# Kernel tuning notes

Measured on AMD Instinct MI355X. Metric: run time of the kernel, lower is better.

The kernel has to match this reference:

```python
import jax, jax.numpy as jnp
import numpy as np

SEG_LEN = 64
SIG_LEN = 1056
NUM_SEG = 32
STEP = 32  # segment_length * (1 - overlap)

# flat scatter indices: position of element j of segment i in the output signal
_IDX = (np.arange(NUM_SEG)[:, None] * STEP + np.arange(SEG_LEN)[None, :]).reshape(-1)


def combine_segments(segments):
    # segments: (B, C, NUM_SEG, SEG_LEN) -> (B, C, SIG_LEN) overlap-add then normalize
    B, C = segments.shape[0], segments.shape[1]
    idx = jnp.asarray(_IDX)
    out = jnp.zeros((B, C, SIG_LEN), segments.dtype).at[:, :, idx].add(
        segments.reshape(B, C, NUM_SEG * SEG_LEN))
    counter = jnp.zeros((SIG_LEN,), segments.dtype).at[idx].add(1.0)
    return out / counter  # broadcast over (B, C)


def setup_inputs() -> dict:
    key = jax.random.key(0)
    ks = jax.random.split(key, 9)
    B, C, T, E, H = 1024, 8, 32, 128, 256
    s = lambda k, shape, fan: jax.random.normal(k, shape, jnp.float32) * (1.0 / np.sqrt(fan))
    return {
        "encoder_output": jax.random.normal(ks[0], (B, C, T, E), jnp.float32),
        "W1": s(ks[1], (H, E), E), "b1": s(ks[2], (H,), E),
        "W2": s(ks[3], (E, H), H), "b2": s(ks[4], (E,), H),
        "Winv": s(ks[5], (SEG_LEN, E), E), "binv": s(ks[6], (SEG_LEN,), E),
        "Wconv": s(ks[7], (1, C, 3), C * 3), "bconv": s(ks[8], (1,), C * 3),
    }


def reference(encoder_output, W1, b1, W2, b2, Winv, binv, Wconv, bconv):
    # MLP: Linear -> ReLU -> Linear over embedding dim
    h = jax.nn.relu(jnp.einsum('bcte,he->bcth', encoder_output, W1) + b1)
    x = jnp.einsum('bcth,eh->bcte', h, W2) + b2
    # inverse token embedding: E -> SEG_LEN
    x = jnp.einsum('bcte,se->bcts', x, Winv) + binv  # (B, C, T, SEG_LEN)
    # overlap-add reconstruction + normalization
    x = combine_segments(x)  # (B, C, SIG_LEN)
    # ChannelMerger: Conv1d(C -> 1, k=3, padding=1)
    y = jax.lax.conv_general_dilated(
        x, Wconv, window_strides=(1,), padding=[(1, 1)],
        dimension_numbers=('NCH', 'OIH', 'NCH'))
    return y + bconv[None, :, None]
```

## Files before the change

### kernel.cpp

```cpp
#include <hip/hip_runtime.h>
#include <hip/hip_bf16.h>


typedef __bf16 bf16x8 __attribute__((ext_vector_type(8)));
typedef float  f32x4  __attribute__((ext_vector_type(4)));
typedef unsigned int u32;
typedef u32 u32x2 __attribute__((ext_vector_type(2)));

#define L_W1   0
#define L_HS   65536
#define L_SGA  102400
#define L_SGB  119424
#define L_B1   136448
#define L_BC   137472
#define L_WV   137728
#define LDS_SZ 137856

#define BAR_LDS() do {                                              \
    __builtin_amdgcn_sched_barrier(0);                              \
    asm volatile("s_waitcnt lgkmcnt(0)" ::: "memory");              \
    __builtin_amdgcn_s_barrier();                                   \
    __builtin_amdgcn_sched_barrier(0);                              \
  } while (0)

static __device__ __forceinline__ bf16x8 cvt8(f32x4 a, f32x4 b) {
  bf16x8 r;
  r[0] = (__bf16)a[0]; r[1] = (__bf16)a[1]; r[2] = (__bf16)a[2]; r[3] = (__bf16)a[3];
  r[4] = (__bf16)b[0]; r[5] = (__bf16)b[1]; r[6] = (__bf16)b[2]; r[7] = (__bf16)b[3];
  return r;
}
static __device__ __forceinline__ u32 packbf2(float a, float b) {
  union { __hip_bfloat16 h; unsigned short s; } ua, ub;
  ua.h = __float2bfloat16(a); ub.h = __float2bfloat16(b);
  return (u32)ua.s | ((u32)ub.s << 16);
}
static __device__ __forceinline__ float lo16f(u32 w) { return __uint_as_float(w << 16); }
static __device__ __forceinline__ float hi16f(u32 w) { return __uint_as_float(w & 0xffff0000u); }

__global__ __launch_bounds__(256) void k_precomp(
    const float* __restrict__ W2, const float* __restrict__ b2,
    const float* __restrict__ Winv, const float* __restrict__ binv,
    __hip_bfloat16* __restrict__ Wcpre, float* __restrict__ bc) {
  __shared__ float wrow[128];
  const int s = blockIdx.x, h = threadIdx.x;
  if (h < 128) wrow[h] = Winv[s * 128 + h];
  __syncthreads();
  float acc = 0.f;
  #pragma unroll 8
  for (int e = 0; e < 128; ++e) acc = fmaf(wrow[e], W2[e * 256 + h], acc);
  const int nc = h >> 6, ks2 = (h >> 5) & 1, g = (h >> 3) & 3, j = h & 7;
  const int nt2 = s >> 4, q = s & 15;
  Wcpre[((((nc * 2 + ks2) * 4 + nt2) * 4 + g) * 16 + q) * 8 + j] = __float2bfloat16(acc);
  if (h == 0) {
    float a = binv[s];
    for (int e = 0; e < 128; ++e) a = fmaf(wrow[e], b2[e], a);
    bc[s] = a;
  }
}

__global__ __launch_bounds__(512)
__attribute__((amdgpu_waves_per_eu(2, 2)))
void k_gemm(const float* __restrict__ X,
            const float* __restrict__ W1,
            const float* __restrict__ b1,
            const __hip_bfloat16* __restrict__ Wcpre,
            const float* __restrict__ bcp,
            const float* __restrict__ Wcv,
            const float* __restrict__ bcv,
            float* __restrict__ Out)
{
  extern __shared__ __align__(16) char smem[];
  const int tid = threadIdx.x;
  const int wave = tid >> 6, lane = tid & 63;
  const int q = lane & 15, g = lane >> 4;
  const int c = wave;
  const int b0 = blockIdx.x * 4;

  f32x4 xa[16];
  #define LOADX(bb) do {                                                        \
    _Pragma("unroll")                                                           \
    for (int _mt = 0; _mt < 2; ++_mt) {                                         \
      const float* _s = X + ((size_t)((bb) * 8 + c)) * 4096                     \
                          + (_mt * 16 + q) * 128 + g * 8;                       \
      _Pragma("unroll")                                                         \
      for (int _ks = 0; _ks < 4; ++_ks) {                                       \
        xa[(_mt * 4 + _ks) * 2 + 0] = *reinterpret_cast<const f32x4*>(_s + _ks * 32);     \
        xa[(_mt * 4 + _ks) * 2 + 1] = *reinterpret_cast<const f32x4*>(_s + _ks * 32 + 4); \
      } } } while (0)

  LOADX(b0);

  #pragma unroll
  for (int i = 0; i < 8; ++i) {
    const int p8 = tid + i * 512;
    const int fq = p8 & 15, fg = (p8 >> 4) & 3, fks = (p8 >> 6) & 3;
    const int fnt = (p8 >> 8) & 3, fnc = (p8 >> 10) & 3;
    const float* src = W1 + (fnc * 64 + fnt * 16 + fq) * 128 + fks * 32 + fg * 8;
    *reinterpret_cast<bf16x8*>(smem + L_W1 + p8 * 16) =
        cvt8(*reinterpret_cast<const f32x4*>(src),
             *reinterpret_cast<const f32x4*>(src + 4));
  }
  {
    if (tid < 256)               ((float*)(smem + L_B1))[tid]       = b1[tid];
    if (tid >= 256 && tid < 320) ((float*)(smem + L_BC))[tid - 256] = bcp[tid - 256];
    if (tid >= 320 && tid < 344) ((float*)(smem + L_WV))[tid - 320] = Wcv[tid - 320];
    if (tid == 344)              ((float*)(smem + L_WV))[24]        = bcv[0];
    if (tid >= 384 && tid < 448) {
      const int t = tid - 384, buf = t >> 5, cc = (t & 31) >> 2, k = t & 3;
      *reinterpret_cast<u32*>(
          reinterpret_cast<__hip_bfloat16*>(smem + (buf ? L_SGB : L_SGA))
          + cc * 1064 + 1056 + 2 * k) = 0u;
    }
  }
  BAR_LDS();

  __hip_bfloat16* Hb = reinterpret_cast<__hip_bfloat16*>(smem + L_HS) + wave * 2304;
  const float* smB1 = (const float*)(smem + L_B1);
  const float* smBC = (const float*)(smem + L_BC);
  const float* smWV = (const float*)(smem + L_WV);

  #pragma unroll 1
  for (int it = 0; it < 4; ++it) {
    bf16x8 af[2][4];
    #pragma unroll
    for (int f = 0; f < 8; ++f) af[f >> 2][f & 3] = cvt8(xa[2 * f], xa[2 * f + 1]);

    f32x4 acc2[2][4] = {};

    #pragma unroll 1
    for (int nc = 0; nc < 4; ++nc) {
      bf16x8 bw2f[2][4];
      #pragma unroll
      for (int ks2 = 0; ks2 < 2; ++ks2)
        #pragma unroll
        for (int nt2 = 0; nt2 < 4; ++nt2)
          bw2f[ks2][nt2] = *reinterpret_cast<const bf16x8*>(
              Wcpre + ((nc * 2 + ks2) * 4 + nt2) * 512 + lane * 8);

      f32x4 acc1[2][4] = {};
      #pragma unroll
      for (int ks = 0; ks < 4; ++ks) {
        bf16x8 bw[4];
        #pragma unroll
        for (int nt = 0; nt < 4; ++nt)
          bw[nt] = *reinterpret_cast<const bf16x8*>(
              smem + L_W1 + (((nc * 4 + nt) * 4 + ks) << 10) + lane * 16);
        __builtin_amdgcn_s_setprio(1);
        #pragma unroll
        for (int nt = 0; nt < 4; ++nt) {
          acc1[0][nt] = __builtin_amdgcn_mfma_f32_16x16x32_bf16(bw[nt], af[0][ks], acc1[0][nt], 0, 0, 0);
          acc1[1][nt] = __builtin_amdgcn_mfma_f32_16x16x32_bf16(bw[nt], af[1][ks], acc1[1][nt], 0, 0, 0);
        }
        __builtin_amdgcn_s_setprio(0);
      }
      #pragma unroll
      for (int nt = 0; nt < 4; ++nt) {
        const f32x4 b1q = *reinterpret_cast<const f32x4*>(smB1 + nc * 64 + nt * 16 + 4 * g);
        #pragma unroll
        for (int mt = 0; mt < 2; ++mt) {
          u32x2 w;
          w[0] = packbf2(fmaxf(acc1[mt][nt][0] + b1q[0], 0.f),
                         fmaxf(acc1[mt][nt][1] + b1q[1], 0.f));
          w[1] = packbf2(fmaxf(acc1[mt][nt][2] + b1q[2], 0.f),
                         fmaxf(acc1[mt][nt][3] + b1q[3], 0.f));
          *reinterpret_cast<u32x2*>(Hb + (mt * 16 + q) * 72 + nt * 16 + 4 * g) = w;
        }
      }
      #pragma unroll
      for (int ks2 = 0; ks2 < 2; ++ks2) {
        bf16x8 bh[2];
        #pragma unroll
        for (int mt = 0; mt < 2; ++mt)
          bh[mt] = *reinterpret_cast<const bf16x8*>(Hb + (mt * 16 + q) * 72 + ks2 * 32 + g * 8);
        __builtin_amdgcn_s_setprio(1);
        #pragma unroll
        for (int nt2 = 0; nt2 < 4; ++nt2) {
          acc2[0][nt2] = __builtin_amdgcn_mfma_f32_16x16x32_bf16(bw2f[ks2][nt2], bh[0], acc2[0][nt2], 0, 0, 0);
          acc2[1][nt2] = __builtin_amdgcn_mfma_f32_16x16x32_bf16(bw2f[ks2][nt2], bh[1], acc2[1][nt2], 0, 0, 0);
        }
        __builtin_amdgcn_s_setprio(0);
      }
    }

    if (it < 3) LOADX(b0 + it + 1);

    __hip_bfloat16* Sl = Hb;
    #pragma unroll
    for (int nt2 = 0; nt2 < 4; ++nt2) {
      const f32x4 bcq = *reinterpret_cast<const f32x4*>(smBC + nt2 * 16 + 4 * g);
      #pragma unroll
      for (int mt = 0; mt < 2; ++mt) {
        u32x2 w;
        w[0] = packbf2(acc2[mt][nt2][0] + bcq[0], acc2[mt][nt2][1] + bcq[1]);
        w[1] = packbf2(acc2[mt][nt2][2] + bcq[2], acc2[mt][nt2][3] + bcq[3]);
        *reinterpret_cast<u32x2*>(Sl + (mt * 16 + q) * 68 + nt2 * 16 + 4 * g) = w;
      }
    }

    {
      __hip_bfloat16* sigc = reinterpret_cast<__hip_bfloat16*>(
          smem + ((it & 1) ? L_SGB : L_SGA)) + c * 1064;
      #pragma unroll
      for (int w = 0; w < 5; ++w) {
        const int u = w * 64 + lane;
        if (u < 264) {
          const int p = 4 * u, t = p >> 5, j = p & 31;
          u32x2 r1 = {0u, 0u}, r2 = {0u, 0u};
          if (t < 32) r1 = *reinterpret_cast<const u32x2*>(Sl + t * 68 + j);
          if (t > 0)  r2 = *reinterpret_cast<const u32x2*>(Sl + (t - 1) * 68 + j + 32);
          const float nrm = (t == 0 || t == 32) ? 1.f : 0.5f;
          u32x2 wv;
          wv[0] = packbf2(nrm * (lo16f(r1[0]) + lo16f(r2[0])),
                          nrm * (hi16f(r1[0]) + hi16f(r2[0])));
          wv[1] = packbf2(nrm * (lo16f(r1[1]) + lo16f(r2[1])),
                          nrm * (hi16f(r1[1]) + hi16f(r2[1])));
          *reinterpret_cast<u32x2*>(sigc + p) = wv;
        }
      }
    }

    if (it & 1) {
      BAR_LDS();
      const float bconv = smWV[24];
      #pragma unroll 1
      for (int rr = 0; rr < 2; ++rr) {
        const int u = tid + rr * 512;
        if (u < 528) {
          const int half = (u >= 264) ? 1 : 0;
          const __hip_bfloat16* sg = reinterpret_cast<const __hip_bfloat16*>(
              smem + (half ? L_SGB : L_SGA));
          const int p0 = (u - half * 264) * 4;
          f32x4 acc = {bconv, bconv, bconv, bconv};
          #pragma unroll
          for (int cc = 0; cc < 8; ++cc) {
            const __hip_bfloat16* row = sg + cc * 1064;
            const u32 wm = (p0 > 0) ? *reinterpret_cast<const u32*>(row + p0 - 2) : 0u;
            const u32x2 wc = *reinterpret_cast<const u32x2*>(row + p0);
            const u32 wr = *reinterpret_cast<const u32*>(row + p0 + 4);
            const float l  = hi16f(wm);
            const float a0 = lo16f(wc[0]), a1 = hi16f(wc[0]);
            const float a2 = lo16f(wc[1]), a3 = hi16f(wc[1]);
            const float r  = lo16f(wr);
            const float w0 = smWV[cc * 3], w1 = smWV[cc * 3 + 1], w2 = smWV[cc * 3 + 2];
            acc[0] = fmaf(w0, l,  fmaf(w1, a0, fmaf(w2, a1, acc[0])));
            acc[1] = fmaf(w0, a0, fmaf(w1, a1, fmaf(w2, a2, acc[1])));
            acc[2] = fmaf(w0, a1, fmaf(w1, a2, fmaf(w2, a3, acc[2])));
            acc[3] = fmaf(w0, a2, fmaf(w1, a3, fmaf(w2, r,  acc[3])));
          }
          *reinterpret_cast<f32x4*>(
              Out + (size_t)(b0 + it - 1 + half) * 1056 + p0) = acc;
        }
      }
      if (it != 3) BAR_LDS();
    }
  }
  #undef LOADX
}

extern "C" void kernel_launch(void* const* d_in, const int* in_sizes, int n_in,
                              void* d_out, int out_size, void* d_ws, size_t ws_size,
                              hipStream_t stream) {
  const float* X    = (const float*)d_in[0];
  const float* W1   = (const float*)d_in[1];
  const float* b1   = (const float*)d_in[2];
  const float* W2   = (const float*)d_in[3];
  const float* b2   = (const float*)d_in[4];
  const float* Winv = (const float*)d_in[5];
  const float* binv = (const float*)d_in[6];
  const float* Wcv  = (const float*)d_in[7];
  const float* bcv  = (const float*)d_in[8];

  __hip_bfloat16* Wcpre = (__hip_bfloat16*)((char*)d_ws + 65536);
  float*          bcp   = (float*)((char*)d_ws + 98304);

  k_precomp<<<64, 256, 0, stream>>>(W2, b2, Winv, binv, Wcpre, bcp);
  k_gemm<<<256, 512, LDS_SZ, stream>>>(X, W1, b1, Wcpre, bcp, Wcv, bcv,
                                       (float*)d_out);
}
```

Before: 58.96 us.

## Split fused GEMM into small-block GEMM plus separate conv kernel via workspace

Replaces the single large-LDS 512-thread kernel (256 blocks, one per 4 batches) with a 2048-block kernel that does MLP+projection+overlap-add per (batch, half of channels) and writes the bf16 signal to workspace, followed by a separate conv kernel. W1 is pre-converted to bf16 in MFMA fragment order in the precompute kernel and read directly from global/L2 instead of staged in LDS. The aim is to raise occupancy and parallelism by dropping the large LDS footprint and cross-channel synchronization, at the cost of an extra kernel launch, an intermediate bf16 round-trip through memory, and an additional bf16 rounding of the signal. The old fused path stays as a fallback when the workspace is too small.

```diff
diff --git a/kernel.cpp b/kernel.cpp
--- a/kernel.cpp
+++ b/kernel.cpp
@@ -16,6 +16,11 @@
 #define L_WV   137728
 #define LDS_SZ 137856
 
+#define LA_HS  0
+#define LA_B1  18432
+#define LA_BC  19456
+#define LA_SZ  19712
+
 #define BAR_LDS() do {                                              \
     __builtin_amdgcn_sched_barrier(0);                              \
     asm volatile("s_waitcnt lgkmcnt(0)" ::: "memory");              \
@@ -38,11 +43,22 @@
 static __device__ __forceinline__ float hi16f(u32 w) { return __uint_as_float(w & 0xffff0000u); }
 
 __global__ __launch_bounds__(256) void k_precomp(
+    const float* __restrict__ W1,
     const float* __restrict__ W2, const float* __restrict__ b2,
     const float* __restrict__ Winv, const float* __restrict__ binv,
-    __hip_bfloat16* __restrict__ Wcpre, float* __restrict__ bc) {
+    __hip_bfloat16* __restrict__ Wcpre, __hip_bfloat16* __restrict__ W1pre,
+    float* __restrict__ bc) {
   __shared__ float wrow[128];
   const int s = blockIdx.x, h = threadIdx.x;
+  if (h < 64) {
+    const int p8 = s * 64 + h;
+    const int fq = p8 & 15, fg = (p8 >> 4) & 3, fks = (p8 >> 6) & 3;
+    const int fnt = (p8 >> 8) & 3, fnc = (p8 >> 10) & 3;
+    const float* src = W1 + (fnc * 64 + fnt * 16 + fq) * 128 + fks * 32 + fg * 8;
+    *reinterpret_cast<bf16x8*>(W1pre + p8 * 8) =
+        cvt8(*reinterpret_cast<const f32x4*>(src),
+             *reinterpret_cast<const f32x4*>(src + 4));
+  }
   if (h < 128) wrow[h] = Winv[s * 128 + h];
   __syncthreads();
   float acc = 0.f;
@@ -58,17 +74,182 @@
   }
 }
 
+__global__ __launch_bounds__(256)
+void k_gemm_s(const float* __restrict__ X,
+              const __hip_bfloat16* __restrict__ W1p,
+              const float* __restrict__ b1,
+              const __hip_bfloat16* __restrict__ Wcpre,
+              const float* __restrict__ bcp,
+              __hip_bfloat16* __restrict__ Sig)
+{
+  __shared__ __align__(16) char smem[LA_SZ];
+  const int tid = threadIdx.x;
+  const int wave = tid >> 6, lane = tid & 63;
+  const int q = lane & 15, g = lane >> 4;
+  const int b = blockIdx.x >> 1, cq = blockIdx.x & 1;
+  const int c = cq * 4 + wave;
+
+  f32x4 xa[16];
+  {
+    const float* xs = X + ((size_t)(b * 8 + c)) * 4096;
+    #pragma unroll
+    for (int mt = 0; mt < 2; ++mt)
+      #pragma unroll
+      for (int ks = 0; ks < 4; ++ks) {
+        const float* s = xs + (mt * 16 + q) * 128 + ks * 32 + g * 8;
+        xa[(mt * 4 + ks) * 2 + 0] = *reinterpret_cast<const f32x4*>(s);
+        xa[(mt * 4 + ks) * 2 + 1] = *reinterpret_cast<const f32x4*>(s + 4);
+      }
+  }
+
+  if (tid < 256) ((float*)(smem + LA_B1))[tid] = b1[tid];
+  if (tid < 64)  ((float*)(smem + LA_BC))[tid] = bcp[tid];
+  BAR_LDS();
+
+  __hip_bfloat16* Hb = reinterpret_cast<__hip_bfloat16*>(smem + LA_HS) + wave * 2304;
+  const float* smB1 = (const float*)(smem + LA_B1);
+  const float* smBC = (const float*)(smem + LA_BC);
+
+  bf16x8 af[2][4];
+  #pragma unroll
+  for (int f = 0; f < 8; ++f) af[f >> 2][f & 3] = cvt8(xa[2 * f], xa[2 * f + 1]);
+
+  f32x4 acc2[2][4] = {};
+
+  #pragma unroll 1
+  for (int nc = 0; nc < 4; ++nc) {
+    f32x4 acc1[2][4] = {};
+    #pragma unroll
+    for (int ks = 0; ks < 4; ++ks) {
+      bf16x8 bw[4];
+      #pragma unroll
+      for (int nt = 0; nt < 4; ++nt)
+        bw[nt] = *reinterpret_cast<const bf16x8*>(
+            W1p + (((nc * 4 + nt) * 4 + ks) << 9) + lane * 8);
+      __builtin_amdgcn_s_setprio(1);
+      #pragma unroll
+      for (int nt = 0; nt < 4; ++nt) {
+        acc1[0][nt] = __builtin_amdgcn_mfma_f32_16x16x32_bf16(bw[nt], af[0][ks], acc1[0][nt], 0, 0, 0);
+        acc1[1][nt] = __builtin_amdgcn_mfma_f32_16x16x32_bf16(bw[nt], af[1][ks], acc1[1][nt], 0, 0, 0);
+      }
+      __builtin_amdgcn_s_setprio(0);
+    }
+    #pragma unroll
+    for (int nt = 0; nt < 4; ++nt) {
+      const f32x4 b1q = *reinterpret_cast<const f32x4*>(smB1 + nc * 64 + nt * 16 + 4 * g);
+      #pragma unroll
+      for (int mt = 0; mt < 2; ++mt) {
+        u32x2 w;
+        w[0] = packbf2(fmaxf(acc1[mt][nt][0] + b1q[0], 0.f),
+                       fmaxf(acc1[mt][nt][1] + b1q[1], 0.f));
+        w[1] = packbf2(fmaxf(acc1[mt][nt][2] + b1q[2], 0.f),
+                       fmaxf(acc1[mt][nt][3] + b1q[3], 0.f));
+        *reinterpret_cast<u32x2*>(Hb + (mt * 16 + q) * 72 + nt * 16 + 4 * g) = w;
+      }
+    }
+    #pragma unroll
+    for (int ks2 = 0; ks2 < 2; ++ks2) {
+      bf16x8 bh[2];
+      #pragma unroll
+      for (int mt = 0; mt < 2; ++mt)
+        bh[mt] = *reinterpret_cast<const bf16x8*>(Hb + (mt * 16 + q) * 72 + ks2 * 32 + g * 8);
+      bf16x8 bw2[4];
+      #pragma unroll
+      for (int nt2 = 0; nt2 < 4; ++nt2)
+        bw2[nt2] = *reinterpret_cast<const bf16x8*>(
+            Wcpre + ((nc * 2 + ks2) * 4 + nt2) * 512 + lane * 8);
+      __builtin_amdgcn_s_setprio(1);
+      #pragma unroll
+      for (int nt2 = 0; nt2 < 4; ++nt2) {
+        acc2[0][nt2] = __builtin_amdgcn_mfma_f32_16x16x32_bf16(bw2[nt2], bh[0], acc2[0][nt2], 0, 0, 0);
+        acc2[1][nt2] = __builtin_amdgcn_mfma_f32_16x16x32_bf16(bw2[nt2], bh[1], acc2[1][nt2], 0, 0, 0);
+      }
+      __builtin_amdgcn_s_setprio(0);
+    }
+  }
+
+  __hip_bfloat16* Sl = Hb;
+  #pragma unroll
+  for (int nt2 = 0; nt2 < 4; ++nt2) {
+    const f32x4 bcq = *reinterpret_cast<const f32x4*>(smBC + nt2 * 16 + 4 * g);
+    #pragma unroll
+    for (int mt = 0; mt < 2; ++mt) {
+      u32x2 w;
+      w[0] = packbf2(acc2[mt][nt2][0] + bcq[0], acc2[mt][nt2][1] + bcq[1]);
+      w[1] = packbf2(acc2[mt][nt2][2] + bcq[2], acc2[mt][nt2][3] + bcq[3]);
+      *reinterpret_cast<u32x2*>(Sl + (mt * 16 + q) * 68 + nt2 * 16 + 4 * g) = w;
+    }
+  }
+
+  {
+    __hip_bfloat16* sigc = Sig + (size_t)(b * 8 + c) * 1056;
+    #pragma unroll
+    for (int w = 0; w < 5; ++w) {
+      const int u = w * 64 + lane;
+      if (u < 264) {
+        const int p = 4 * u, t = p >> 5, j = p & 31;
+        u32x2 r1 = {0u, 0u}, r2 = {0u, 0u};
+        if (t < 32) r1 = *reinterpret_cast<const u32x2*>(Sl + t * 68 + j);
+        if (t > 0)  r2 = *reinterpret_cast<const u32x2*>(Sl + (t - 1) * 68 + j + 32);
+        const float nrm = (t == 0 || t == 32) ? 1.f : 0.5f;
+        u32x2 wv;
+        wv[0] = packbf2(nrm * (lo16f(r1[0]) + lo16f(r2[0])),
+                        nrm * (hi16f(r1[0]) + hi16f(r2[0])));
+        wv[1] = packbf2(nrm * (lo16f(r1[1]) + lo16f(r2[1])),
+                        nrm * (hi16f(r1[1]) + hi16f(r2[1])));
+        *reinterpret_cast<u32x2*>(sigc + p) = wv;
+      }
+    }
+  }
+}
+
+__global__ __launch_bounds__(256)
+void k_conv(const __hip_bfloat16* __restrict__ Sig,
+            const float* __restrict__ Wcv, const float* __restrict__ bcv,
+            float* __restrict__ Out) {
+  __shared__ float wv[25];
+  if (threadIdx.x < 24) wv[threadIdx.x] = Wcv[threadIdx.x];
+  if (threadIdx.x == 24) wv[24] = bcv[0];
+  __syncthreads();
+  const int b = blockIdx.x;
+  const float bconv = wv[24];
+  #pragma unroll 1
+  for (int rr = 0; rr < 2; ++rr) {
+    const int u = threadIdx.x + rr * 256;
+    if (u < 264) {
+      const int p0 = 4 * u;
+      f32x4 acc = {bconv, bconv, bconv, bconv};
+      #pragma unroll
+      for (int cc = 0; cc < 8; ++cc) {
+        const __hip_bfloat16* row = Sig + (size_t)(b * 8 + cc) * 1056;
+        const u32 wm = (p0 > 0) ? *reinterpret_cast<const u32*>(row + p0 - 2) : 0u;
+        const u32x2 wc = *reinterpret_cast<const u32x2*>(row + p0);
+        const u32 wr = (p0 + 4 < 1056) ? *reinterpret_cast<const u32*>(row + p0 + 4) : 0u;
+        const float l  = hi16f(wm);
+        const float a0 = lo16f(wc[0]), a1 = hi16f(wc[0]);
+        const float a2 = lo16f(wc[1]), a3 = hi16f(wc[1]);
+        const float r  = lo16f(wr);
+        const float w0 = wv[cc * 3], w1 = wv[cc * 3 + 1], w2 = wv[cc * 3 + 2];
+        acc[0] = fmaf(w0, l,  fmaf(w1, a0, fmaf(w2, a1, acc[0])));
+        acc[1] = fmaf(w0, a0, fmaf(w1, a1, fmaf(w2, a2, acc[1])));
+        acc[2] = fmaf(w0, a1, fmaf(w1, a2, fmaf(w2, a3, acc[2])));
+        acc[3] = fmaf(w0, a2, fmaf(w1, a3, fmaf(w2, r,  acc[3])));
+      }
+      *reinterpret_cast<f32x4*>(Out + (size_t)b * 1056 + p0) = acc;
+    }
+  }
+}
+
 __global__ __launch_bounds__(512)
 __attribute__((amdgpu_waves_per_eu(2, 2)))
-void k_gemm(const float* __restrict__ X,
-            const float* __restrict__ W1,
-            const float* __restrict__ b1,
-            const __hip_bfloat16* __restrict__ Wcpre,
-            const float* __restrict__ bcp,
-            const float* __restrict__ Wcv,
-            const float* __restrict__ bcv,
-            float* __restrict__ Out)
-{
+void k_gemm_fused(const float* __restrict__ X,
+                  const float* __restrict__ W1,
+                  const float* __restrict__ b1,
+                  const __hip_bfloat16* __restrict__ Wcpre,
+                  const float* __restrict__ bcp,
+                  const float* __restrict__ Wcv,
+                  const float* __restrict__ bcv,
+                  float* __restrict__ Out) {
   extern __shared__ __align__(16) char smem[];
   const int tid = threadIdx.x;
   const int wave = tid >> 6, lane = tid & 63;
@@ -270,10 +451,18 @@
   const float* Wcv  = (const float*)d_in[7];
   const float* bcv  = (const float*)d_in[8];
 
+  __hip_bfloat16* W1pre = (__hip_bfloat16*)d_ws;
   __hip_bfloat16* Wcpre = (__hip_bfloat16*)((char*)d_ws + 65536);
   float*          bcp   = (float*)((char*)d_ws + 98304);
-
-  k_precomp<<<64, 256, 0, stream>>>(W2, b2, Winv, binv, Wcpre, bcp);
-  k_gemm<<<256, 512, LDS_SZ, stream>>>(X, W1, b1, Wcpre, bcp, Wcv, bcv,
-                                       (float*)d_out);
-}
+  __hip_bfloat16* Sig   = (__hip_bfloat16*)((char*)d_ws + 131072);
+  const size_t need = 131072 + (size_t)1024 * 8 * 1056 * 2;
+
+  k_precomp<<<64, 256, 0, stream>>>(W1, W2, b2, Winv, binv, Wcpre, W1pre, bcp);
+  if (ws_size >= need) {
+    k_gemm_s<<<2048, 256, 0, stream>>>(X, W1pre, b1, Wcpre, bcp, Sig);
+    k_conv<<<1024, 256, 0, stream>>>(Sig, Wcv, bcv, (float*)d_out);
+  } else {
+    k_gemm_fused<<<256, 512, LDS_SZ, stream>>>(X, W1, b1, Wcpre, bcp, Wcv, bcv,
+                                               (float*)d_out);
+  }
+}
```

New measurement: 83.40 us. 41.4% more time.

## Software-pipeline fused MLP chunk loop to overlap GEMM1 of next chunk with GEMM2

Applied to the files above, without the earlier changes.

Restructures the per-chunk hidden-dimension loop into a software pipeline: the H tile for chunk nc is written and read back, then GEMM1 for chunk nc+1 is issued before GEMM2 for chunk nc, and the W2 fragments for the next chunk are prefetched afterwards. The aim is to hide the LDS write/read latency of the hidden activations and the global W2 loads behind independent MFMA work. In exchange, more accumulators and fragments are live at once, which raises register pressure and could reduce occupancy or cause spills.

```diff
diff --git a/kernel.cpp b/kernel.cpp
--- a/kernel.cpp
+++ b/kernel.cpp
@@ -119,6 +119,77 @@
   const float* smBC = (const float*)(smem + L_BC);
   const float* smWV = (const float*)(smem + L_WV);
 
+  #define LOADW2(ncx) do {                                                      \
+    _Pragma("unroll")                                                           \
+    for (int _k = 0; _k < 2; ++_k)                                              \
+      _Pragma("unroll")                                                         \
+      for (int _n = 0; _n < 4; ++_n)                                            \
+        bw2f[_k][_n] = *reinterpret_cast<const bf16x8*>(                        \
+            Wcpre + (((ncx) * 2 + _k) * 4 + _n) * 512 + lane * 8);              \
+  } while (0)
+
+  #define GEMM1(ncx) do {                                                       \
+    _Pragma("unroll")                                                           \
+    for (int _m = 0; _m < 2; ++_m)                                              \
+      _Pragma("unroll")                                                         \
+      for (int _n = 0; _n < 4; ++_n)                                            \
+        acc1[_m][_n] = (f32x4){0.f, 0.f, 0.f, 0.f};                             \
+    _Pragma("unroll")                                                           \
+    for (int _ks = 0; _ks < 4; ++_ks) {                                         \
+      bf16x8 _bw[4];                                                            \
+      _Pragma("unroll")                                                         \
+      for (int _n = 0; _n < 4; ++_n)                                            \
+        _bw[_n] = *reinterpret_cast<const bf16x8*>(                             \
+            smem + L_W1 + ((((ncx) * 4 + _n) * 4 + _ks) << 10) + lane * 16);    \
+      __builtin_amdgcn_s_setprio(1);                                            \
+      _Pragma("unroll")                                                         \
+      for (int _n = 0; _n < 4; ++_n) {                                          \
+        acc1[0][_n] = __builtin_amdgcn_mfma_f32_16x16x32_bf16(_bw[_n], af[0][_ks], acc1[0][_n], 0, 0, 0); \
+        acc1[1][_n] = __builtin_amdgcn_mfma_f32_16x16x32_bf16(_bw[_n], af[1][_ks], acc1[1][_n], 0, 0, 0); \
+      }                                                                         \
+      __builtin_amdgcn_s_setprio(0);                                            \
+    }                                                                           \
+  } while (0)
+
+  #define HWRITE(ncx) do {                                                      \
+    _Pragma("unroll")                                                           \
+    for (int _n = 0; _n < 4; ++_n) {                                            \
+      const f32x4 _b1q = *reinterpret_cast<const f32x4*>(                       \
+          smB1 + (ncx) * 64 + _n * 16 + 4 * g);                                 \
+      _Pragma("unroll")                                                         \
+      for (int _m = 0; _m < 2; ++_m) {                                          \
+        u32x2 _w;                                                               \
+        _w[0] = packbf2(fmaxf(acc1[_m][_n][0] + _b1q[0], 0.f),                  \
+                        fmaxf(acc1[_m][_n][1] + _b1q[1], 0.f));                 \
+        _w[1] = packbf2(fmaxf(acc1[_m][_n][2] + _b1q[2], 0.f),                  \
+                        fmaxf(acc1[_m][_n][3] + _b1q[3], 0.f));                 \
+        *reinterpret_cast<u32x2*>(Hb + (_m * 16 + q) * 72 + _n * 16 + 4 * g) = _w; \
+      }                                                                         \
+    }                                                                           \
+  } while (0)
+
+  #define BHREAD() do {                                                         \
+    _Pragma("unroll")                                                           \
+    for (int _k = 0; _k < 2; ++_k)                                              \
+      _Pragma("unroll")                                                         \
+      for (int _m = 0; _m < 2; ++_m)                                            \
+        bh[_k][_m] = *reinterpret_cast<const bf16x8*>(                          \
+            Hb + (_m * 16 + q) * 72 + _k * 32 + g * 8);                         \
+  } while (0)
+
+  #define GEMM2() do {                                                          \
+    _Pragma("unroll")                                                           \
+    for (int _k = 0; _k < 2; ++_k) {                                            \
+      __builtin_amdgcn_s_setprio(1);                                            \
+      _Pragma("unroll")                                                         \
+      for (int _n = 0; _n < 4; ++_n) {                                          \
+        acc2[0][_n] = __builtin_amdgcn_mfma_f32_16x16x32_bf16(bw2f[_k][_n], bh[_k][0], acc2[0][_n], 0, 0, 0); \
+        acc2[1][_n] = __builtin_amdgcn_mfma_f32_16x16x32_bf16(bw2f[_k][_n], bh[_k][1], acc2[1][_n], 0, 0, 0); \
+      }                                                                         \
+      __builtin_amdgcn_s_setprio(0);                                            \
+    }                                                                           \
+  } while (0)
+
   #pragma unroll 1
   for (int it = 0; it < 4; ++it) {
     bf16x8 af[2][4];
@@ -126,61 +197,24 @@
     for (int f = 0; f < 8; ++f) af[f >> 2][f & 3] = cvt8(xa[2 * f], xa[2 * f + 1]);
 
     f32x4 acc2[2][4] = {};
+    f32x4 acc1[2][4];
+    bf16x8 bw2f[2][4];
+    bf16x8 bh[2][2];
+
+    LOADW2(0);
+    GEMM1(0);
 
     #pragma unroll 1
-    for (int nc = 0; nc < 4; ++nc) {
-      bf16x8 bw2f[2][4];
-      #pragma unroll
-      for (int ks2 = 0; ks2 < 2; ++ks2)
-        #pragma unroll
-        for (int nt2 = 0; nt2 < 4; ++nt2)
-          bw2f[ks2][nt2] = *reinterpret_cast<const bf16x8*>(
-              Wcpre + ((nc * 2 + ks2) * 4 + nt2) * 512 + lane * 8);
-
-      f32x4 acc1[2][4] = {};
-      #pragma unroll
-      for (int ks = 0; ks < 4; ++ks) {
-        bf16x8 bw[4];
-        #pragma unroll
-        for (int nt = 0; nt < 4; ++nt)
-          bw[nt] = *reinterpret_cast<const bf16x8*>(
-              smem + L_W1 + (((nc * 4 + nt) * 4 + ks) << 10) + lane * 16);
-        __builtin_amdgcn_s_setprio(1);
-        #pragma unroll
-        for (int nt = 0; nt < 4; ++nt) {
-          acc1[0][nt] = __builtin_amdgcn_mfma_f32_16x16x32_bf16(bw[nt], af[0][ks], acc1[0][nt], 0, 0, 0);
-          acc1[1][nt] = __builtin_amdgcn_mfma_f32_16x16x32_bf16(bw[nt], af[1][ks], acc1[1][nt], 0, 0, 0);
-        }
-        __builtin_amdgcn_s_setprio(0);
-      }
-      #pragma unroll
-      for (int nt = 0; nt < 4; ++nt) {
-        const f32x4 b1q = *reinterpret_cast<const f32x4*>(smB1 + nc * 64 + nt * 16 + 4 * g);
-        #pragma unroll
-        for (int mt = 0; mt < 2; ++mt) {
-          u32x2 w;
-          w[0] = packbf2(fmaxf(acc1[mt][nt][0] + b1q[0], 0.f),
-                         fmaxf(acc1[mt][nt][1] + b1q[1], 0.f));
-          w[1] = packbf2(fmaxf(acc1[mt][nt][2] + b1q[2], 0.f),
-                         fmaxf(acc1[mt][nt][3] + b1q[3], 0.f));
-          *reinterpret_cast<u32x2*>(Hb + (mt * 16 + q) * 72 + nt * 16 + 4 * g) = w;
-        }
-      }
-      #pragma unroll
-      for (int ks2 = 0; ks2 < 2; ++ks2) {
-        bf16x8 bh[2];
-        #pragma unroll
-        for (int mt = 0; mt < 2; ++mt)
-          bh[mt] = *reinterpret_cast<const bf16x8*>(Hb + (mt * 16 + q) * 72 + ks2 * 32 + g * 8);
-        __builtin_amdgcn_s_setprio(1);
-        #pragma unroll
-        for (int nt2 = 0; nt2 < 4; ++nt2) {
-          acc2[0][nt2] = __builtin_amdgcn_mfma_f32_16x16x32_bf16(bw2f[ks2][nt2], bh[0], acc2[0][nt2], 0, 0, 0);
-          acc2[1][nt2] = __builtin_amdgcn_mfma_f32_16x16x32_bf16(bw2f[ks2][nt2], bh[1], acc2[1][nt2], 0, 0, 0);
-        }
-        __builtin_amdgcn_s_setprio(0);
-      }
-    }
+    for (int nc = 0; nc < 3; ++nc) {
+      HWRITE(nc);
+      BHREAD();
+      GEMM1(nc + 1);
+      GEMM2();
+      LOADW2(nc + 1);
+    }
+    HWRITE(3);
+    BHREAD();
+    GEMM2();
 
     if (it < 3) LOADX(b0 + it + 1);
 
@@ -255,6 +289,11 @@
     }
   }
   #undef LOADX
+  #undef LOADW2
+  #undef GEMM1
+  #undef HWRITE
+  #undef BHREAD
+  #undef GEMM2
 }
 
 extern "C" void kernel_launch(void* const* d_in, const int* in_sizes, int n_in,
```

After: 73.75 us. 1.25x slower.
